# Optimization experiments

Measured on AMD Instinct MI355X. Metric: run time of the kernel, lower is better.

Reference implementation:

```python
import jax, jax.numpy as jnp
import numpy as np

B, C, H, T_IN, T, EPS = 2048, 512, 256, 64, 32, 1e-5


def _interp_linear(x, t_out):
    # torch F.interpolate mode='linear', align_corners=False on [B,C,T]
    t_in = x.shape[-1]
    scale = t_in / t_out
    src = jnp.maximum((jnp.arange(t_out, dtype=jnp.float32) + 0.5) * scale - 0.5, 0.0)
    i0 = jnp.minimum(jnp.floor(src).astype(jnp.int32), t_in - 1)
    i1 = jnp.minimum(i0 + 1, t_in - 1)
    w1 = (src - i0.astype(jnp.float32))
    return x[:, :, i0] * (1.0 - w1) + x[:, :, i1] * w1


def _dwconv(x, w, pad):
    # depthwise conv1d: x [B,C,T], w [C,1,K]
    return jax.lax.conv_general_dilated(
        x, w, window_strides=(1,), padding=[(pad, pad)],
        dimension_numbers=('NCH', 'OIH', 'NCH'), feature_group_count=x.shape[1])


def _bn(x, g, b, m, v):  # eval-mode BatchNorm1d over channel dim of [B,C,T]
    inv = g / jnp.sqrt(v + EPS)
    return (x - m[:, None]) * inv[:, None] + b[:, None]


def _ln(x, g, b):  # LayerNorm over last dim
    mu = x.mean(-1, keepdims=True)
    var = x.var(-1, keepdims=True)
    return (x - mu) / jnp.sqrt(var + EPS) * g + b


def _gelu(x):
    return jax.nn.gelu(x, approximate=False)


def _attn_weights(feats, lg, lb, w1, b1, w2, b2, temp):
    h = _gelu(_ln(feats, lg, lb) @ w1.T + b1)          # [B,T,H]
    s = (h @ w2.T + b2) / jnp.clip(temp, 0.25, 4.0)    # [B,T,1]
    return jax.nn.softmax(s, axis=1)


def setup_inputs() -> dict:
    key = jax.random.key(0)
    ks = jax.random.split(key, 40)
    n = lambda i, shape, s=0.02: jax.random.normal(ks[i], shape, jnp.float32) * s
    u = lambda i, shape: jax.random.uniform(ks[i], shape, jnp.float32, 0.5, 1.5)
    inp = {
        'x': jax.random.normal(ks[0], (B, C, T_IN), jnp.float32),
        'pos_embed': n(1, (1, T, C)),
        'w3': n(2, (C, 1, 3), 0.1),
        'bn3_g': u(3, (C,)), 'bn3_b': n(4, (C,)), 'bn3_m': n(5, (C,)), 'bn3_v': u(6, (C,)),
        'w5': n(7, (C, 1, 5), 0.1),
        'bn5_g': u(8, (C,)), 'bn5_b': n(9, (C,)), 'bn5_m': n(10, (C,)), 'bn5_v': u(11, (C,)),
        'wmix': n(12, (C, 3 * C), 0.02),
        'bnm_g': u(13, (C,)), 'bnm_b': n(14, (C,)), 'bnm_m': n(15, (C,)), 'bnm_v': u(16, (C,)),
        'ln_g': u(17, (C,)), 'ln_b': n(18, (C,)),
        'ed_ln_g': u(19, (C,)), 'ed_ln_b': n(20, (C,)),
        'ed_w1': n(21, (H, C), 0.04), 'ed_b1': n(22, (H,)),
        'ed_w2': n(23, (1, H), 0.06), 'ed_b2': n(24, (1,)),
        'es_ln_g': u(25, (C,)), 'es_ln_b': n(26, (C,)),
        'es_w1': n(27, (H, C), 0.04), 'es_b1': n(28, (H,)),
        'es_w2': n(29, (1, H), 0.06), 'es_b2': n(30, (1,)),
        'temp_ed': jnp.float32(1.0), 'temp_es': jnp.float32(1.0),
    }
    return inp


def reference(x, pos_embed, w3, bn3_g, bn3_b, bn3_m, bn3_v, w5, bn5_g, bn5_b, bn5_m, bn5_v,
              wmix, bnm_g, bnm_b, bnm_m, bnm_v, ln_g, ln_b,
              ed_ln_g, ed_ln_b, ed_w1, ed_b1, ed_w2, ed_b2,
              es_ln_g, es_ln_b, es_w1, es_b1, es_w2, es_b2, temp_ed, temp_es):
    tf = _interp_linear(x, T)                                 # [B,C,T]
    c3 = _gelu(_bn(_dwconv(tf, w3, 1), bn3_g, bn3_b, bn3_m, bn3_v))
    c5 = _gelu(_bn(_dwconv(tf, w5, 2), bn5_g, bn5_b, bn5_m, bn5_v))
    cat = jnp.concatenate([tf, c3, c5], axis=1)               # [B,3C,T]
    ctx = _gelu(_bn(jnp.einsum('bct,oc->bot', cat, wmix), bnm_g, bnm_b, bnm_m, bnm_v))
    feats = _ln(tf.transpose(0, 2, 1) + ctx.transpose(0, 2, 1) + pos_embed, ln_g, ln_b)  # [B,T,C]
    aw_ed = _attn_weights(feats, ed_ln_g, ed_ln_b, ed_w1, ed_b1, ed_w2, ed_b2, temp_ed)
    aw_es = _attn_weights(feats, es_ln_g, es_ln_b, es_w1, es_b1, es_w2, es_b2, temp_es)
    pair = jnp.concatenate([aw_ed, aw_es], axis=-1)           # [B,T,2]
    w_mean = pair.mean(axis=-1, keepdims=True)                # [B,T,1]
    pooled = (feats * w_mean).sum(axis=1)                     # [B,C]
    return feats, pooled, pair
```

## Files before the change

### kernel.cpp

```cpp
#include <hip/hip_runtime.h>
#include <cstdint>

typedef __bf16 bf16;
typedef __attribute__((ext_vector_type(8))) __bf16 bf16x8;
typedef __attribute__((ext_vector_type(4))) float f32x4;

#define CEPS 1e-5f
#define MROWS 65536
#define NB 2048
#define CDIM 512
#define K3C 1536

__device__ __forceinline__ float gelu_f(float x) {
  float x2 = x * x;
  float u = x * (0.7978845608f + 0.0356774081f * x2);
  float e = __expf(2.0f * u);
  float th = 1.0f - __fdividef(2.0f, e + 1.0f);
  return 0.5f * x * (1.0f + th);
}

__device__ __forceinline__ void gload_lds16(const void* g, void* l) {
  using GP = const __attribute__((address_space(1))) void*;
  using LP = __attribute__((address_space(3))) void*;
  __builtin_amdgcn_global_load_lds(reinterpret_cast<GP>(reinterpret_cast<uintptr_t>(g)),
                                   reinterpret_cast<LP>(reinterpret_cast<uintptr_t>(l)),
                                   16, 0, 0);
}

__global__ __launch_bounds__(256) void fold_kernel(
    const float* __restrict__ wmix, const float* __restrict__ bnm_g, const float* __restrict__ bnm_v,
    const float* __restrict__ edg, const float* __restrict__ edb,
    const float* __restrict__ esg, const float* __restrict__ esb,
    const float* __restrict__ w1a, const float* __restrict__ w1b,
    const float* __restrict__ b1a, const float* __restrict__ b1b,
    bf16* __restrict__ wmixf, bf16* __restrict__ w1f, float* __restrict__ b1f) {
  __shared__ float red[4];
  int bid = blockIdx.x, tid = threadIdx.x;
  if (bid < 512) {
    int o = bid;
    float s = bnm_g[o] * rsqrtf(bnm_v[o] + CEPS);
    for (int c = tid; c < K3C; c += 256)
      wmixf[(size_t)o * K3C + c] = (bf16)(wmix[(size_t)o * K3C + c] * s);
  } else {
    int n = bid - 512;
    int half = (n < 256) ? 0 : 1;
    const float* g  = half ? esg : edg;
    const float* lb = half ? esb : edb;
    const float* w1 = half ? w1b : w1a;
    const float* b1 = half ? b1b : b1a;
    int nn = n & 255;
    float dot = 0.f;
    for (int c = tid; c < 512; c += 256) {
      float w = w1[(size_t)nn * 512 + c];
      w1f[(size_t)n * 512 + c] = (bf16)(w * g[c]);
      dot += w * lb[c];
    }
    #pragma unroll
    for (int off = 1; off < 64; off <<= 1) dot += __shfl_xor(dot, off, 64);
    if ((tid & 63) == 0) red[tid >> 6] = dot;
    __syncthreads();
    if (tid == 0) b1f[n] = b1[nn] + red[0] + red[1] + red[2] + red[3];
  }
}

__global__ __launch_bounds__(512) void prep_kernel(
    const float* __restrict__ x,
    const float* __restrict__ w3, const float* __restrict__ bn3g, const float* __restrict__ bn3b,
    const float* __restrict__ bn3m, const float* __restrict__ bn3v,
    const float* __restrict__ w5, const float* __restrict__ bn5g, const float* __restrict__ bn5b,
    const float* __restrict__ bn5m, const float* __restrict__ bn5v,
    bf16* __restrict__ Acat) {
  int b = blockIdx.x, c = threadIdx.x;
  const float4* xp = (const float4*)(x + ((size_t)b * 512 + c) * 64);
  float tf[32];
  #pragma unroll
  for (int i = 0; i < 16; i++) {
    float4 v = xp[i];
    tf[2 * i]     = 0.5f * (v.x + v.y);
    tf[2 * i + 1] = 0.5f * (v.z + v.w);
  }
  float s3 = bn3g[c] * rsqrtf(bn3v[c] + CEPS), t3 = bn3b[c] - bn3m[c] * s3;
  float s5 = bn5g[c] * rsqrtf(bn5v[c] + CEPS), t5 = bn5b[c] - bn5m[c] * s5;
  float w30 = w3[c * 3], w31 = w3[c * 3 + 1], w32 = w3[c * 3 + 2];
  float w50 = w5[c * 5], w51 = w5[c * 5 + 1], w52 = w5[c * 5 + 2], w53 = w5[c * 5 + 3], w54 = w5[c * 5 + 4];
  bf16* Ab = Acat + (size_t)b * 32 * K3C + c;
  #pragma unroll
  for (int t = 0; t < 32; t++) {
    float tm2 = (t >= 2) ? tf[t - 2] : 0.f;
    float tm1 = (t >= 1) ? tf[t - 1] : 0.f;
    float tp1 = (t < 31) ? tf[t + 1] : 0.f;
    float tp2 = (t < 30) ? tf[t + 2] : 0.f;
    float c3 = gelu_f((w30 * tm1 + w31 * tf[t] + w32 * tp1) * s3 + t3);
    float c5 = gelu_f((w50 * tm2 + w51 * tm1 + w52 * tf[t] + w53 * tp1 + w54 * tp2) * s5 + t5);
    Ab[t * K3C]        = (bf16)tf[t];
    Ab[t * K3C + 512]  = (bf16)c3;
    Ab[t * K3C + 1024] = (bf16)c5;
  }
}

#define GBM 256
#define GBN 256
#define GBK 64

__device__ __forceinline__ int xcd_swz(int bid, int nwg) {
  int q = nwg >> 3, r = nwg & 7;
  int xcd = bid & 7, i = bid >> 3;
  return (xcd < r ? xcd * (q + 1) : r * (q + 1) + (xcd - r) * q) + i;
}

#define BARRIER_SB()  do { __builtin_amdgcn_s_barrier(); __builtin_amdgcn_sched_barrier(0); } while (0)

#define LOAD_A(q)                                                     \
  bf16x8 Af[2][2];                                                    \
  _Pragma("unroll")                                                   \
  for (int im = 0; im < 2; im++)                                      \
    _Pragma("unroll")                                                 \
    for (int k2 = 0; k2 < 2; k2++)                                    \
      Af[im][k2] = ldA(s, 2 * (q) + im, k2 * 32);

#define MFMA_Q(q)                                                     \
  __builtin_amdgcn_s_setprio(1);                                      \
  _Pragma("unroll")                                                   \
  for (int k2 = 0; k2 < 2; k2++)                                      \
    _Pragma("unroll")                                                 \
    for (int im = 0; im < 2; im++)                                    \
      _Pragma("unroll")                                               \
      for (int nr = 0; nr < 4; nr++)                                  \
        acc[2 * (q) + im][nr] = __builtin_amdgcn_mfma_f32_16x16x32_bf16( \
            Af[im][k2], Bf[nr][k2], acc[2 * (q) + im][nr], 0, 0, 0);  \
  __builtin_amdgcn_s_setprio(0);

template <int EPI, int KC>
__global__ __launch_bounds__(512, 2) void gemm8(
    const bf16* __restrict__ A, const bf16* __restrict__ Bm, bf16* __restrict__ out,
    float* __restrict__ sE, float* __restrict__ sS,
    const float* __restrict__ bn_g, const float* __restrict__ bn_b,
    const float* __restrict__ bn_m, const float* __restrict__ bn_v,
    const float* __restrict__ b1f,
    const float* __restrict__ w2a, const float* __restrict__ w2b,
    const float* __restrict__ ta, const float* __restrict__ tb) {
  __shared__ char lds[131072];
  constexpr int KB = KC * 2;
  constexpr int kt = KC / GBK;
  int tid = threadIdx.x;
  int wv = tid >> 6, lane = tid & 63;
  int wm = wv >> 2, wn = wv & 3;
  int fr = lane & 15, kq = lane >> 4;
  int wgid = xcd_swz(blockIdx.x, gridDim.x);
  int mb = wgid >> 1, nb = wgid & 1;

  const bf16* Ag = A + (size_t)mb * GBM * KC;
  const bf16* Bg = Bm + (size_t)nb * GBN * KC;

  auto stage_half = [&](const bf16* Gsrc, int k0, int ldsoff) {
    #pragma unroll
    for (int l = 0; l < 2; l++) {
      int p = l * 8192 + tid * 16;
      int r = p >> 7;
      int sc = (p & 127) ^ ((r & 7) << 4);
      const char* g = (const char*)Gsrc + (size_t)r * KB + k0 * 2 + sc;
      gload_lds16(g, lds + ldsoff + l * 8192 + wv * 1024);
    }
  };
  auto ldA = [&](int s, int mr, int kk) -> bf16x8 {
    int rr = mr * 16 + fr;
    int off = s * 65536 + wm * 16384 + ((rr * 128 + kk * 2 + kq * 16) ^ ((rr & 7) << 4));
    return *(const bf16x8*)(lds + off);
  };
  auto ldB = [&](int s, int nr, int kk) -> bf16x8 {
    int row = wn * 64 + nr * 16 + fr;
    int off = s * 65536 + 32768 + ((row >> 7) * 16384)
            + (((row & 127) * 128 + kk * 2 + kq * 16) ^ ((row & 7) << 4));
    return *(const bf16x8*)(lds + off);
  };

  const f32x4 fz = {0.f, 0.f, 0.f, 0.f};
  f32x4 acc[8][4];
  #pragma unroll
  for (int i = 0; i < 8; i++)
    #pragma unroll
    for (int j = 0; j < 4; j++) acc[i][j] = fz;

  stage_half(Ag,            0,   0);
  stage_half(Ag + 128 * KC, 0,   16384);
  stage_half(Bg,            0,   32768);
  stage_half(Bg + 128 * KC, 0,   49152);
  stage_half(Bg,            GBK, 65536 + 32768);
  stage_half(Bg + 128 * KC, GBK, 65536 + 49152);
  asm volatile("s_waitcnt vmcnt(4)" ::: "memory");
  BARRIER_SB();

  for (int t = 0; t < kt; t++) {
    int s = t & 1;
    bf16x8 Bf[4][2];
    if (t + 1 < kt) stage_half(Ag, (t + 1) * GBK, (s ^ 1) * 65536);
    #pragma unroll
    for (int nr = 0; nr < 4; nr++)
      #pragma unroll
      for (int k2 = 0; k2 < 2; k2++) Bf[nr][k2] = ldB(s, nr, k2 * 32);
    {
      LOAD_A(0);
      BARRIER_SB();
      MFMA_Q(0);
    }
    BARRIER_SB();
    if (t + 1 < kt) stage_half(Ag + 128 * KC, (t + 1) * GBK, (s ^ 1) * 65536 + 16384);
    {
      LOAD_A(1);
      BARRIER_SB();
      MFMA_Q(1);
    }
    BARRIER_SB();
    if (t + 2 < kt) stage_half(Bg, (t + 2) * GBK, s * 65536 + 32768);
    {
      LOAD_A(2);
      BARRIER_SB();
      MFMA_Q(2);
    }
    BARRIER_SB();
    if (t + 2 < kt) stage_half(Bg + 128 * KC, (t + 2) * GBK, s * 65536 + 49152);
    {
      LOAD_A(3);
      BARRIER_SB();
      MFMA_Q(3);
    }
    if (t < kt - 2) {
      asm volatile("s_waitcnt vmcnt(4)" ::: "memory");
    } else if (t == kt - 2) {
      asm volatile("s_waitcnt vmcnt(0)" ::: "memory");
    }
    BARRIER_SB();
  }

  if constexpr (EPI == 0) {
    #pragma unroll
    for (int nr = 0; nr < 4; nr++) {
      int n = nb * GBN + wn * 64 + nr * 16 + fr;
      float sc = bn_g[n] * rsqrtf(bn_v[n] + CEPS);
      float bias = bn_b[n] - bn_m[n] * sc;
      #pragma unroll
      for (int mr = 0; mr < 8; mr++)
        #pragma unroll
        for (int j = 0; j < 4; j++) {
          size_t m = (size_t)mb * GBM + wm * 128 + mr * 16 + kq * 4 + j;
          out[m * CDIM + n] = (bf16)gelu_f(acc[mr][nr][j] + bias);
        }
    }
  } else {
    float bias[4], w2s[4];
    #pragma unroll
    for (int nr = 0; nr < 4; nr++) {
      int n = nb * GBN + wn * 64 + nr * 16 + fr;
      bias[nr] = b1f[n];
      float tv = (n < 256) ? ta[0] : tb[0];
      tv = fminf(fmaxf(tv, 0.25f), 4.0f);
      w2s[nr] = ((n < 256) ? w2a[n] : w2b[n - 256]) / tv;
    }
    float* sred = (float*)lds;
    __syncthreads();
    #pragma unroll
    for (int mr = 0; mr < 8; mr++) {
      float p0 = 0.f, p1 = 0.f, p2 = 0.f, p3 = 0.f;
      #pragma unroll
      for (int nr = 0; nr < 4; nr++) {
        p0 += gelu_f(acc[mr][nr][0] + bias[nr]) * w2s[nr];
        p1 += gelu_f(acc[mr][nr][1] + bias[nr]) * w2s[nr];
        p2 += gelu_f(acc[mr][nr][2] + bias[nr]) * w2s[nr];
        p3 += gelu_f(acc[mr][nr][3] + bias[nr]) * w2s[nr];
      }
      #pragma unroll
      for (int off = 1; off < 16; off <<= 1) {
        p0 += __shfl_xor(p0, off, 64);
        p1 += __shfl_xor(p1, off, 64);
        p2 += __shfl_xor(p2, off, 64);
        p3 += __shfl_xor(p3, off, 64);
      }
      if (fr == 0) {
        int rbase = wm * 128 + mr * 16 + kq * 4;
        sred[wn * 256 + rbase]     = p0;
        sred[wn * 256 + rbase + 1] = p1;
        sred[wn * 256 + rbase + 2] = p2;
        sred[wn * 256 + rbase + 3] = p3;
      }
    }
    __syncthreads();
    if (tid < 256) {
      float sv = sred[tid] + sred[256 + tid] + sred[512 + tid] + sred[768 + tid];
      float* so = nb ? sS : sE;
      so[(size_t)mb * GBM + tid] = sv;
    }
  }
}

__global__ __launch_bounds__(256) void ln_kernel(
    const bf16* __restrict__ Acat, const bf16* __restrict__ ctx, const float* __restrict__ pos,
    const float* __restrict__ lng, const float* __restrict__ lnb,
    float* __restrict__ feats, bf16* __restrict__ zhat) {
  int m = blockIdx.x * 4 + (threadIdx.x >> 6);
  int lane = threadIdx.x & 63;
  int c0 = lane * 8;
  int t = m & 31;
  bf16x8 tf8 = *(const bf16x8*)(Acat + (size_t)m * K3C + c0);
  bf16x8 cx8 = *(const bf16x8*)(ctx + (size_t)m * 512 + c0);
  const float* pp = pos + t * 512 + c0;
  float z[8], s = 0.f, ss = 0.f;
  #pragma unroll
  for (int j = 0; j < 8; j++) {
    z[j] = (float)tf8[j] + (float)cx8[j] + pp[j];
    s += z[j]; ss += z[j] * z[j];
  }
  #pragma unroll
  for (int off = 1; off < 64; off <<= 1) { s += __shfl_xor(s, off, 64); ss += __shfl_xor(ss, off, 64); }
  float mu = s * (1.f / 512.f);
  float var = ss * (1.f / 512.f) - mu * mu;
  float inv = rsqrtf(var + CEPS);
  float f[8], s2 = 0.f, ss2 = 0.f;
  #pragma unroll
  for (int j = 0; j < 8; j++) {
    f[j] = (z[j] - mu) * inv * lng[c0 + j] + lnb[c0 + j];
    s2 += f[j]; ss2 += f[j] * f[j];
  }
  float4* fo = (float4*)(feats + (size_t)m * 512 + c0);
  fo[0] = make_float4(f[0], f[1], f[2], f[3]);
  fo[1] = make_float4(f[4], f[5], f[6], f[7]);
  #pragma unroll
  for (int off = 1; off < 64; off <<= 1) { s2 += __shfl_xor(s2, off, 64); ss2 += __shfl_xor(ss2, off, 64); }
  float mu2 = s2 * (1.f / 512.f);
  float var2 = ss2 * (1.f / 512.f) - mu2 * mu2;
  float inv2 = rsqrtf(var2 + CEPS);
  bf16x8 zv;
  #pragma unroll
  for (int j = 0; j < 8; j++) zv[j] = (bf16)((f[j] - mu2) * inv2);
  *(bf16x8*)(zhat + (size_t)m * 512 + c0) = zv;
}

__global__ __launch_bounds__(256) void final_kernel(
    const float* __restrict__ sE, const float* __restrict__ sS,
    const float* __restrict__ feats, float* __restrict__ pair, float* __restrict__ pooled) {
  __shared__ float wmL[32];
  int b = blockIdx.x, tid = threadIdx.x;
  if (tid < 32) {
    float vE = sE[(size_t)b * 32 + tid], vS = sS[(size_t)b * 32 + tid];
    float mE = vE, mS = vS;
    #pragma unroll
    for (int off = 1; off < 32; off <<= 1) {
      mE = fmaxf(mE, __shfl_xor(mE, off, 32));
      mS = fmaxf(mS, __shfl_xor(mS, off, 32));
    }
    float eE = expf(vE - mE), eS = expf(vS - mS);
    float sumE = eE, sumS = eS;
    #pragma unroll
    for (int off = 1; off < 32; off <<= 1) {
      sumE += __shfl_xor(sumE, off, 32);
      sumS += __shfl_xor(sumS, off, 32);
    }
    float awE = eE / sumE, awS = eS / sumS;
    size_t pidx = ((size_t)b * 32 + tid) * 2;
    pair[pidx] = awE;
    pair[pidx + 1] = awS;
    wmL[tid] = 0.5f * (awE + awS);
  }
  __syncthreads();
  {
    int c = tid * 2;
    float a0 = 0.f, a1 = 0.f;
    #pragma unroll
    for (int t = 0; t < 32; t++) {
      float2 v = *(const float2*)&feats[((size_t)b * 32 + t) * 512 + c];
      float w = wmL[t];
      a0 += v.x * w; a1 += v.y * w;
    }
    *(float2*)&pooled[(size_t)b * 512 + c] = make_float2(a0, a1);
  }
}

extern "C" void kernel_launch(void* const* d_in, const int* in_sizes, int n_in,
                              void* d_out, int out_size, void* d_ws, size_t ws_size,
                              hipStream_t stream) {
  const float* x     = (const float*)d_in[0];
  const float* pos   = (const float*)d_in[1];
  const float* w3    = (const float*)d_in[2];
  const float* bn3g  = (const float*)d_in[3];
  const float* bn3b  = (const float*)d_in[4];
  const float* bn3m  = (const float*)d_in[5];
  const float* bn3v  = (const float*)d_in[6];
  const float* w5    = (const float*)d_in[7];
  const float* bn5g  = (const float*)d_in[8];
  const float* bn5b  = (const float*)d_in[9];
  const float* bn5m  = (const float*)d_in[10];
  const float* bn5v  = (const float*)d_in[11];
  const float* wmix  = (const float*)d_in[12];
  const float* bnmg  = (const float*)d_in[13];
  const float* bnmb  = (const float*)d_in[14];
  const float* bnmm  = (const float*)d_in[15];
  const float* bnmv  = (const float*)d_in[16];
  const float* lng   = (const float*)d_in[17];
  const float* lnb   = (const float*)d_in[18];
  const float* edlng = (const float*)d_in[19];
  const float* edlnb = (const float*)d_in[20];
  const float* edw1  = (const float*)d_in[21];
  const float* edb1  = (const float*)d_in[22];
  const float* edw2  = (const float*)d_in[23];
  const float* eslng = (const float*)d_in[25];
  const float* eslnb = (const float*)d_in[26];
  const float* esw1  = (const float*)d_in[27];
  const float* esb1  = (const float*)d_in[28];
  const float* esw2  = (const float*)d_in[29];
  const float* ted   = (const float*)d_in[31];
  const float* tes   = (const float*)d_in[32];

  char* ws = (char*)d_ws;
  bf16* Acat  = (bf16*)ws;
  bf16* ctx   = (bf16*)(ws + 201326592);
  bf16* zhat  = (bf16*)(ws + 268435456);
  bf16* wmixf = (bf16*)(ws + 335544320);
  bf16* w1f   = (bf16*)(ws + 337117184);
  float* b1f  = (float*)(ws + 337641472);
  float* sEb  = (float*)ws;
  float* sSb  = (float*)(ws + 262144);

  float* feats  = (float*)d_out;
  float* pooled = feats + 33554432;
  float* pair   = pooled + 1048576;

  fold_kernel<<<1024, 256, 0, stream>>>(wmix, bnmg, bnmv, edlng, edlnb, eslng, eslnb,
                                        edw1, esw1, edb1, esb1, wmixf, w1f, b1f);
  prep_kernel<<<NB, 512, 0, stream>>>(x, w3, bn3g, bn3b, bn3m, bn3v,
                                      w5, bn5g, bn5b, bn5m, bn5v, Acat);
  gemm8<0, K3C><<<(MROWS / GBM) * (CDIM / GBN), 512, 0, stream>>>(
      Acat, wmixf, ctx, nullptr, nullptr,
      bnmg, bnmb, bnmm, bnmv, nullptr, nullptr, nullptr, nullptr, nullptr);
  ln_kernel<<<MROWS / 4, 256, 0, stream>>>(Acat, ctx, pos, lng, lnb, feats, zhat);
  gemm8<1, CDIM><<<(MROWS / GBM) * (CDIM / GBN), 512, 0, stream>>>(
      zhat, w1f, nullptr, sEb, sSb,
      nullptr, nullptr, nullptr, nullptr, b1f, edw2, esw2, ted, tes);
  final_kernel<<<NB, 256, 0, stream>>>(sEb, sSb, feats, pair, pooled);
}
```

Before: 407.7 us.

## Precompute LDS/global addresses and stage GEMM epilogue through LDS for vector stores

The GEMM main loop now precomputes the swizzled LDS read offsets and the global staging pointers once, then advances the pointers by a constant each k-step instead of recomputing addresses inside lambdas. The barrier macro loses its sched_barrier, which gives the compiler more freedom to reorder around barriers. The EPI==0 epilogue writes the GELU output into a swizzled LDS tile and then copies it out with coalesced 16-byte global stores, replacing scattered 2-byte writes. This costs an extra __syncthreads and LDS traffic, and dropping sched_barrier risks the compiler interleaving instructions differently than intended.

```diff
diff --git a/kernel.cpp b/kernel.cpp
--- a/kernel.cpp
+++ b/kernel.cpp
@@ -108,16 +108,6 @@
   return (xcd < r ? xcd * (q + 1) : r * (q + 1) + (xcd - r) * q) + i;
 }
 
-#define BARRIER_SB()  do { __builtin_amdgcn_s_barrier(); __builtin_amdgcn_sched_barrier(0); } while (0)
-
-#define LOAD_A(q)                                                     \
-  bf16x8 Af[2][2];                                                    \
-  _Pragma("unroll")                                                   \
-  for (int im = 0; im < 2; im++)                                      \
-    _Pragma("unroll")                                                 \
-    for (int k2 = 0; k2 < 2; k2++)                                    \
-      Af[im][k2] = ldA(s, 2 * (q) + im, k2 * 32);
-
 #define MFMA_Q(q)                                                     \
   __builtin_amdgcn_s_setprio(1);                                      \
   _Pragma("unroll")                                                   \
@@ -129,6 +119,14 @@
         acc[2 * (q) + im][nr] = __builtin_amdgcn_mfma_f32_16x16x32_bf16( \
             Af[im][k2], Bf[nr][k2], acc[2 * (q) + im][nr], 0, 0, 0);  \
   __builtin_amdgcn_s_setprio(0);
+
+#define LOAD_A(q)                                                     \
+  bf16x8 Af[2][2];                                                    \
+  _Pragma("unroll")                                                   \
+  for (int im = 0; im < 2; im++) {                                    \
+    Af[im][0] = *(const bf16x8*)(LA0 + (2 * (q) + im) * 2048);        \
+    Af[im][1] = *(const bf16x8*)(LA1 + (2 * (q) + im) * 2048);        \
+  }
 
 template <int EPI, int KC>
 __global__ __launch_bounds__(512, 2) void gemm8(
@@ -152,27 +150,18 @@
   const bf16* Ag = A + (size_t)mb * GBM * KC;
   const bf16* Bg = Bm + (size_t)nb * GBN * KC;
 
-  auto stage_half = [&](const bf16* Gsrc, int k0, int ldsoff) {
-    #pragma unroll
-    for (int l = 0; l < 2; l++) {
-      int p = l * 8192 + tid * 16;
-      int r = p >> 7;
-      int sc = (p & 127) ^ ((r & 7) << 4);
-      const char* g = (const char*)Gsrc + (size_t)r * KB + k0 * 2 + sc;
-      gload_lds16(g, lds + ldsoff + l * 8192 + wv * 1024);
-    }
-  };
-  auto ldA = [&](int s, int mr, int kk) -> bf16x8 {
-    int rr = mr * 16 + fr;
-    int off = s * 65536 + wm * 16384 + ((rr * 128 + kk * 2 + kq * 16) ^ ((rr & 7) << 4));
-    return *(const bf16x8*)(lds + off);
-  };
-  auto ldB = [&](int s, int nr, int kk) -> bf16x8 {
-    int row = wn * 64 + nr * 16 + fr;
-    int off = s * 65536 + 32768 + ((row >> 7) * 16384)
-            + (((row & 127) * 128 + kk * 2 + kq * 16) ^ ((row & 7) << 4));
-    return *(const bf16x8*)(lds + off);
-  };
+  int r0 = tid >> 3;
+  int sc0 = ((tid & 7) << 4) ^ ((r0 & 7) << 4);
+  const char* sAp = (const char*)Ag + (size_t)r0 * KB + sc0;
+  const char* sBp = (const char*)Bg + (size_t)r0 * KB + sc0;
+  const int wv1024 = wv * 1024;
+
+  int ek0 = (kq << 4) ^ ((fr & 7) << 4);
+  int ek1 = (64 | (kq << 4)) ^ ((fr & 7) << 4);
+  int aB = wm * 16384 + fr * 128;
+  int bB = 32768 + (wn >> 1) * 16384 + (((wn & 1) * 64 + fr) * 128);
+  const int a0 = aB + ek0, a1 = aB + ek1;
+  const int b0 = bB + ek0, b1 = bB + ek1;
 
   const f32x4 fz = {0.f, 0.f, 0.f, 0.f};
   f32x4 acc[8][4];
@@ -181,47 +170,65 @@
     #pragma unroll
     for (int j = 0; j < 4; j++) acc[i][j] = fz;
 
-  stage_half(Ag,            0,   0);
-  stage_half(Ag + 128 * KC, 0,   16384);
-  stage_half(Bg,            0,   32768);
-  stage_half(Bg + 128 * KC, 0,   49152);
-  stage_half(Bg,            GBK, 65536 + 32768);
-  stage_half(Bg + 128 * KC, GBK, 65536 + 49152);
+  {
+    char* d = lds + wv1024;
+    gload_lds16(sAp,               d);
+    gload_lds16(sAp + 64 * KB,     d + 8192);
+    gload_lds16(sAp + 128 * KB,    d + 16384);
+    gload_lds16(sAp + 192 * KB,    d + 24576);
+    gload_lds16(sBp,               d + 32768);
+    gload_lds16(sBp + 64 * KB,     d + 40960);
+    gload_lds16(sBp + 128 * KB,    d + 49152);
+    gload_lds16(sBp + 192 * KB,    d + 57344);
+    gload_lds16(sBp + 128,            d + 65536 + 32768);
+    gload_lds16(sBp + 128 + 64 * KB,  d + 65536 + 40960);
+    gload_lds16(sBp + 128 + 128 * KB, d + 65536 + 49152);
+    gload_lds16(sBp + 128 + 192 * KB, d + 65536 + 57344);
+  }
   asm volatile("s_waitcnt vmcnt(4)" ::: "memory");
-  BARRIER_SB();
+  __builtin_amdgcn_s_barrier();
 
   for (int t = 0; t < kt; t++) {
-    int s = t & 1;
+    const int sofs = (t & 1) << 16;
+    const char* LA0 = lds + sofs + a0;
+    const char* LA1 = lds + sofs + a1;
+    const char* LB0 = lds + sofs + b0;
+    const char* LB1 = lds + sofs + b1;
+    char* dA = lds + (sofs ^ 65536) + wv1024;
+    char* dB = lds + sofs + wv1024;
+    const bool stA = (t + 1 < kt), stB = (t + 2 < kt);
     bf16x8 Bf[4][2];
-    if (t + 1 < kt) stage_half(Ag, (t + 1) * GBK, (s ^ 1) * 65536);
-    #pragma unroll
-    for (int nr = 0; nr < 4; nr++)
-      #pragma unroll
-      for (int k2 = 0; k2 < 2; k2++) Bf[nr][k2] = ldB(s, nr, k2 * 32);
+
+    if (stA) { gload_lds16(sAp + 128, dA); gload_lds16(sAp + 128 + 64 * KB, dA + 8192); }
+    #pragma unroll
+    for (int nr = 0; nr < 4; nr++) {
+      Bf[nr][0] = *(const bf16x8*)(LB0 + nr * 2048);
+      Bf[nr][1] = *(const bf16x8*)(LB1 + nr * 2048);
+    }
     {
       LOAD_A(0);
-      BARRIER_SB();
+      __builtin_amdgcn_s_barrier();
       MFMA_Q(0);
     }
-    BARRIER_SB();
-    if (t + 1 < kt) stage_half(Ag + 128 * KC, (t + 1) * GBK, (s ^ 1) * 65536 + 16384);
+    __builtin_amdgcn_s_barrier();
+    if (stA) { gload_lds16(sAp + 128 + 128 * KB, dA + 16384); gload_lds16(sAp + 128 + 192 * KB, dA + 24576); }
     {
       LOAD_A(1);
-      BARRIER_SB();
+      __builtin_amdgcn_s_barrier();
       MFMA_Q(1);
     }
-    BARRIER_SB();
-    if (t + 2 < kt) stage_half(Bg, (t + 2) * GBK, s * 65536 + 32768);
+    __builtin_amdgcn_s_barrier();
+    if (stB) { gload_lds16(sBp + 256, dB + 32768); gload_lds16(sBp + 256 + 64 * KB, dB + 40960); }
     {
       LOAD_A(2);
-      BARRIER_SB();
+      __builtin_amdgcn_s_barrier();
       MFMA_Q(2);
     }
-    BARRIER_SB();
-    if (t + 2 < kt) stage_half(Bg + 128 * KC, (t + 2) * GBK, s * 65536 + 49152);
+    __builtin_amdgcn_s_barrier();
+    if (stB) { gload_lds16(sBp + 256 + 128 * KB, dB + 49152); gload_lds16(sBp + 256 + 192 * KB, dB + 57344); }
     {
       LOAD_A(3);
-      BARRIER_SB();
+      __builtin_amdgcn_s_barrier();
       MFMA_Q(3);
     }
     if (t < kt - 2) {
@@ -229,22 +236,40 @@
     } else if (t == kt - 2) {
       asm volatile("s_waitcnt vmcnt(0)" ::: "memory");
     }
-    BARRIER_SB();
+    __builtin_amdgcn_s_barrier();
+    sAp += 128;
+    sBp += 128;
   }
 
   if constexpr (EPI == 0) {
+    int colb = (wn * 64 + fr) * 2;
     #pragma unroll
     for (int nr = 0; nr < 4; nr++) {
       int n = nb * GBN + wn * 64 + nr * 16 + fr;
       float sc = bn_g[n] * rsqrtf(bn_v[n] + CEPS);
       float bias = bn_b[n] - bn_m[n] * sc;
       #pragma unroll
-      for (int mr = 0; mr < 8; mr++)
+      for (int mr = 0; mr < 8; mr++) {
         #pragma unroll
         for (int j = 0; j < 4; j++) {
-          size_t m = (size_t)mb * GBM + wm * 128 + mr * 16 + kq * 4 + j;
-          out[m * CDIM + n] = (bf16)gelu_f(acc[mr][nr][j] + bias);
+          int row = wm * 128 + mr * 16 + kq * 4 + j;
+          int ad = ((row << 9) + colb + nr * 32) ^ ((row & 15) << 5);
+          *(bf16*)(lds + ad) = (bf16)gelu_f(acc[mr][nr][j] + bias);
         }
+      }
+    }
+    __syncthreads();
+    {
+      int rr = tid >> 5;
+      int ch = tid & 31;
+      size_t gbase = (size_t)(mb * GBM + rr) * CDIM + nb * GBN + ch * 8;
+      #pragma unroll
+      for (int p = 0; p < 16; p++) {
+        int row = p * 16 + rr;
+        int ad = ((row << 9) + ch * 16) ^ ((row & 15) << 5);
+        bf16x8 v = *(const bf16x8*)(lds + ad);
+        *(bf16x8*)(out + gbase + (size_t)p * 16 * CDIM) = v;
+      }
     }
   } else {
     float bias[4], w2s[4];
```

Result: faster. 389.4 us (-4.5%).
